# Performance work log

Measured on AMD Instinct MI355X. Metric: run time of the kernel, lower is better.

The kernel has to match this reference:

```python
import jax, jax.numpy as jnp
import numpy as np

N = 32768
H = 256

def setup_inputs() -> dict:
    key = jax.random.key(0)
    ks = jax.random.split(key, 8)
    def glorot(k, shape):
        fan_in, fan_out = shape
        s = jnp.sqrt(2.0 / (fan_in + fan_out)).astype(jnp.float32)
        return jax.random.normal(k, shape, dtype=jnp.float32) * s
    inp = {
        "x_norm": jax.random.normal(ks[0], (N, 3), dtype=jnp.float32),
        "nu": jnp.ones((1,), dtype=jnp.float32) * 0.01,
        "x_std": jnp.array([0.5, 0.5, 0.5], dtype=jnp.float32),
        "y_std": jnp.array([1.2, 1.2, 1.2, 0.8], dtype=jnp.float32),
        "W0": glorot(ks[1], (3, H)), "b0": jnp.zeros((H,), jnp.float32),
        "W1": glorot(ks[2], (H, H)), "b1": jnp.zeros((H,), jnp.float32),
        "W2": glorot(ks[3], (H, H)), "b2": jnp.zeros((H,), jnp.float32),
        "W3": glorot(ks[4], (H, H)), "b3": jnp.zeros((H,), jnp.float32),
        "W4": glorot(ks[5], (H, 4)), "b4": jnp.zeros((4,), jnp.float32),
    }
    return inp

def reference(x_norm, nu, x_std, y_std, W0, b0, W1, b1, W2, b2, W3, b3, W4, b4):
    # per-point MLP: R^3 -> R^4  (u, v, w, p)
    def f(x):
        h = jnp.tanh(x @ W0 + b0)
        h = jnp.tanh(h @ W1 + b1)
        h = jnp.tanh(h @ W2 + b2)
        h = jnp.tanh(h @ W3 + b3)
        return h @ W4 + b4  # [4]

    # Fused single-pass derivatives (replaces 13 autograd.grad calls):
    J = jax.vmap(jax.jacfwd(f))(x_norm)                 # [N,4,3] first derivs
    Hfull = jax.vmap(jax.jacfwd(jax.jacfwd(f)))(x_norm) # [N,4,3,3]
    Hdiag = jnp.diagonal(Hfull, axis1=2, axis2=3)       # [N,4,3] d2/dxi2 only

    # de-normalization scaling: y_std[y] / x_std[x]^order
    Js = J * y_std[None, :, None] / x_std[None, None, :]
    Hs = Hdiag * y_std[None, :, None] / (x_std[None, None, :] ** 2)

    continuity = Js[:, 0, 0] + Js[:, 1, 1] + Js[:, 2, 2]  # du/dx+dv/dy+dw/dz
    lap = Hs.sum(-1)                                       # [N,4] laplacians
    nu_s = nu[0]
    momentum_x = Js[:, 3, 0] - nu_s * lap[:, 0]
    momentum_y = Js[:, 3, 1] - nu_s * lap[:, 1]
    momentum_z = Js[:, 3, 2] - nu_s * lap[:, 2]

    phy_loss = continuity ** 2 + momentum_x ** 2 + momentum_y ** 2 + momentum_z ** 2
    return phy_loss  # [N], reduction='none' (already squeezed)
```

## Files before the change

### kernel.cpp

```cpp
#include <hip/hip_runtime.h>
#include <stdint.h>

typedef __attribute__((ext_vector_type(8))) _Float16 half8v;
typedef __attribute__((ext_vector_type(16))) float float16v;
typedef __attribute__((ext_vector_type(4))) float float4v;

#define NPTS_WG 32
#define NCH 5

__device__ __forceinline__ int agp(int c, int g, int p) {
    return ((c * 32 + g) * 32 + p) * 8;
}

__device__ __forceinline__ unsigned short f16b(float x) {
    const _Float16 h = (_Float16)x;
    return __builtin_bit_cast(unsigned short, h);
}

__device__ __forceinline__ uint32_t pk2f16(float a, float b) {
    return (uint32_t)f16b(a) | ((uint32_t)f16b(b) << 16);
}

__device__ __forceinline__ float fast_tanh(float z) {
    const float e = __expf(2.0f * z);
    return 1.0f - 2.0f / (e + 1.0f);
}

__global__ void wt_split_kernel(const float* __restrict__ W1, const float* __restrict__ W2,
                                const float* __restrict__ W3, unsigned short* __restrict__ wt)
{
    const int b = blockIdx.x;
    const int L = b >> 4;
    const int ch = b & 15;
    const int k0 = ch * 16;
    const float* W = (L == 0) ? W1 : (L == 1) ? W2 : W3;
    const int j = threadIdx.x;
    const int wv = j >> 5, l31 = j & 31;
    uint32_t hi[16], lo[16];
#pragma unroll
    for (int e = 0; e < 16; ++e) {
        const float x = W[(k0 + e) * 256 + j];
        const unsigned short h = f16b(x);
        const float hf = (float)__builtin_bit_cast(_Float16, h);
        hi[e] = h;
        lo[e] = f16b(x - hf);
    }
#pragma unroll
    for (int part = 0; part < 2; ++part) {
        const uint32_t* src = part ? lo : hi;
        unsigned short* base = wt +
            ((((size_t)(L * 2 + part) * 8 + wv) * 16 + ch) * 64) * 8;
#pragma unroll
        for (int hh = 0; hh < 2; ++hh) {
            uint4 v;
            const uint32_t* s = src + hh * 8;
            v.x = s[0] | (s[1] << 16);
            v.y = s[2] | (s[3] << 16);
            v.z = s[4] | (s[5] << 16);
            v.w = s[6] | (s[7] << 16);
            *(uint4*)(base + (hh * 32 + l31) * 8) = v;
        }
    }
}

__global__ __launch_bounds__(512, 4)
void pinn_mfma(const float* __restrict__ x_norm, const float* __restrict__ nu,
               const float* __restrict__ x_std, const float* __restrict__ y_std,
               const float* __restrict__ W0, const float* __restrict__ b0,
               const float* __restrict__ b1, const float* __restrict__ b2,
               const float* __restrict__ b3, const float* __restrict__ W4,
               const unsigned short* __restrict__ wt, float* __restrict__ out)
{
    __shared__ __align__(16) unsigned char smem[NCH * 32 * 256 * 2];
    unsigned short* AH = (unsigned short*)smem;
    float* part_lds = (float*)smem;
    float* y_lds = (float*)(smem + 16384);

    const int tid = threadIdx.x;
    const int lane = tid & 63;
    const int wv = tid >> 6;
    const int l31 = lane & 31;
    const int hh = lane >> 5;
    const int base_pt = blockIdx.x * NPTS_WG;

    const float xs0 = x_std[0], xs1 = x_std[1], xs2 = x_std[2];
    const float ixs20 = 1.f / (xs0 * xs0);
    const float ixs21 = 1.f / (xs1 * xs1);
    const float ixs22 = 1.f / (xs2 * xs2);

    {
        const int p = tid & 31;
        const int jq = tid >> 5;
        const float x0 = x_norm[(base_pt + p) * 3 + 0];
        const float x1 = x_norm[(base_pt + p) * 3 + 1];
        const float x2 = x_norm[(base_pt + p) * 3 + 2];
#pragma unroll
        for (int hf = 0; hf < 2; ++hf) {
            const int j8 = jq * 16 + hf * 8;
            const int g = 2 * jq + hf;
            float w0r[8], w1r[8], w2r[8], b0r[8];
            *(float4*)&w0r[0] = *(const float4*)&W0[0 * 256 + j8];
            *(float4*)&w0r[4] = *(const float4*)&W0[0 * 256 + j8 + 4];
            *(float4*)&w1r[0] = *(const float4*)&W0[1 * 256 + j8];
            *(float4*)&w1r[4] = *(const float4*)&W0[1 * 256 + j8 + 4];
            *(float4*)&w2r[0] = *(const float4*)&W0[2 * 256 + j8];
            *(float4*)&w2r[4] = *(const float4*)&W0[2 * 256 + j8 + 4];
            *(float4*)&b0r[0] = *(const float4*)&b0[j8];
            *(float4*)&b0r[4] = *(const float4*)&b0[j8 + 4];
            union { unsigned short u[8]; half8v v; } hv[NCH];
#pragma unroll
            for (int e = 0; e < 8; ++e) {
                const float z = b0r[e] + x0 * w0r[e] + x1 * w1r[e] + x2 * w2r[e];
                const float t = fast_tanh(z);
                const float s = 1.f - t * t;
                hv[0].u[e] = f16b(t);
                hv[1].u[e] = f16b(s * w0r[e]);
                hv[2].u[e] = f16b(s * w1r[e]);
                hv[3].u[e] = f16b(s * w2r[e]);
                hv[4].u[e] = f16b(-2.f * t * s *
                    (w0r[e] * w0r[e] * ixs20 + w1r[e] * w1r[e] * ixs21 +
                     w2r[e] * w2r[e] * ixs22));
            }
#pragma unroll
            for (int c = 0; c < NCH; ++c)
                *(half8v*)&AH[agp(c, g, p)] = hv[c].v;
        }
    }
    __syncthreads();

    const float* biases[3] = {b1, b2, b3};
    const int laneq = lane * 8;

#pragma unroll 1
    for (int L = 0; L < 3; ++L) {
        const unsigned short* whL = wt + ((size_t)(L * 2 + 0) * 8 + wv) * 8192 + laneq;
        const unsigned short* wlL = wt + ((size_t)(L * 2 + 1) * 8 + wv) * 8192 + laneq;
        float16v acc[NCH];
#pragma unroll
        for (int c = 0; c < NCH; ++c)
#pragma unroll
            for (int e = 0; e < 16; ++e) acc[c][e] = 0.f;

#pragma unroll
        for (int ch = 0; ch < 16; ++ch) {
            const half8v wh = *(const half8v*)(whL + ch * 512);
            const half8v wl = *(const half8v*)(wlL + ch * 512);
            half8v a[NCH];
            const int g = 2 * ch + hh;
#pragma unroll
            for (int c = 0; c < NCH; ++c)
                a[c] = *(const half8v*)&AH[agp(c, g, l31)];
            __builtin_amdgcn_s_setprio(1);
#pragma unroll
            for (int c = 0; c < NCH; ++c)
                acc[c] = __builtin_amdgcn_mfma_f32_32x32x16_f16(wh, a[c], acc[c], 0, 0, 0);
#pragma unroll
            for (int c = 0; c < 4; ++c)
                acc[c] = __builtin_amdgcn_mfma_f32_32x32x16_f16(wl, a[c], acc[c], 0, 0, 0);
            __builtin_amdgcn_s_setprio(0);
        }

        const float* bL = biases[L];
        __syncthreads();
#pragma unroll
        for (int q = 0; q < 4; ++q) {
            const int j0 = wv * 32 + 8 * q + 4 * hh;
            const int g = wv * 4 + q;
            float bj[4];
            *(float4*)&bj[0] = *(const float4*)&bL[j0];
            float val[NCH][4];
#pragma unroll
            for (int r = 0; r < 4; ++r) {
                const int e = q * 4 + r;
                const float z = acc[0][e] + bj[r];
                const float t = fast_tanh(z);
                const float s = 1.f - t * t;
                const float d1a = acc[1][e], d1b = acc[2][e], d1c = acc[3][e];
                val[0][r] = t;
                val[1][r] = s * d1a;
                val[2][r] = s * d1b;
                val[3][r] = s * d1c;
                val[4][r] = s * acc[4][e] - 2.f * t * s *
                    (d1a * d1a * ixs20 + d1b * d1b * ixs21 + d1c * d1c * ixs22);
            }
#pragma unroll
            for (int c = 0; c < NCH; ++c) {
                const uint32_t u0 = pk2f16(val[c][0], val[c][1]);
                const uint32_t u1 = pk2f16(val[c][2], val[c][3]);
                *(uint2*)&AH[agp(c, g, l31) + 4 * hh] = make_uint2(u0, u1);
            }
        }
        __syncthreads();
    }

    {
        const int l15 = lane & 15;
        const int g4 = lane >> 4;
        const int koct = wv * 32 + 8 * g4;
        const int gr = wv * 4 + g4;
        union { uint32_t u[4]; half8v v; } HB, LB;
#pragma unroll
        for (int i = 0; i < 4; ++i) {
            const float w0v = (l15 < 4) ? W4[(koct + 2 * i) * 4 + l15] : 0.f;
            const float w1v = (l15 < 4) ? W4[(koct + 2 * i + 1) * 4 + l15] : 0.f;
            const unsigned short h0 = f16b(w0v), h1 = f16b(w1v);
            const float r0 = w0v - (float)__builtin_bit_cast(_Float16, h0);
            const float r1 = w1v - (float)__builtin_bit_cast(_Float16, h1);
            HB.u[i] = (uint32_t)h0 | ((uint32_t)h1 << 16);
            LB.u[i] = (uint32_t)f16b(r0) | ((uint32_t)f16b(r1) << 16);
        }
        float4v acc4[4][2];
#pragma unroll
        for (int cc = 0; cc < 4; ++cc)
#pragma unroll
            for (int ph = 0; ph < 2; ++ph) acc4[cc][ph] = (float4v){0.f, 0.f, 0.f, 0.f};
#pragma unroll
        for (int cc = 0; cc < 4; ++cc) {
#pragma unroll
            for (int ph = 0; ph < 2; ++ph) {
                const half8v ah = *(const half8v*)&AH[agp(1 + cc, gr, l15 + 16 * ph)];
                acc4[cc][ph] = __builtin_amdgcn_mfma_f32_16x16x32_f16(HB.v, ah, acc4[cc][ph], 0, 0, 0);
                if (cc < 3)
                    acc4[cc][ph] = __builtin_amdgcn_mfma_f32_16x16x32_f16(LB.v, ah, acc4[cc][ph], 0, 0, 0);
            }
        }
        __syncthreads();
        if (g4 == 0) {
#pragma unroll
            for (int cc = 0; cc < 4; ++cc)
#pragma unroll
                for (int ph = 0; ph < 2; ++ph)
                    *(float4*)&part_lds[((wv * 4 + cc) * 32 + ph * 16 + l15) * 4] =
                        make_float4(acc4[cc][ph][0], acc4[cc][ph][1],
                                    acc4[cc][ph][2], acc4[cc][ph][3]);
        }
    }
    __syncthreads();

    {
        const int p = tid & 31;
        const int co = tid >> 5;
        const int o = co & 3;
        const int c4 = co >> 2;
        float sum = 0.f;
#pragma unroll
        for (int w8 = 0; w8 < 8; ++w8)
            sum += part_lds[((w8 * 4 + c4) * 32 + p) * 4 + o];
        const float scale = (c4 < 3) ? (y_std[o] / x_std[c4]) : y_std[o];
        y_lds[co * 32 + p] = sum * scale;
    }
    __syncthreads();

    if (tid < 32) {
        const int p = tid;
        const float nuv = nu[0];
        #define YV(c4, o) y_lds[(((c4) * 4) + (o)) * 32 + p]
        const float cont = YV(0, 0) + YV(1, 1) + YV(2, 2);
        const float mx = YV(0, 3) - nuv * YV(3, 0);
        const float my = YV(1, 3) - nuv * YV(3, 1);
        const float mz = YV(2, 3) - nuv * YV(3, 2);
        out[base_pt + p] = cont * cont + mx * mx + my * my + mz * mz;
        #undef YV
    }
}

extern "C" void kernel_launch(void* const* d_in, const int* in_sizes, int n_in,
                              void* d_out, int out_size, void* d_ws, size_t ws_size,
                              hipStream_t stream)
{
    const float* x_norm = (const float*)d_in[0];
    const float* nu     = (const float*)d_in[1];
    const float* x_std  = (const float*)d_in[2];
    const float* y_std  = (const float*)d_in[3];
    const float* W0 = (const float*)d_in[4];  const float* b0 = (const float*)d_in[5];
    const float* W1 = (const float*)d_in[6];  const float* b1 = (const float*)d_in[7];
    const float* W2 = (const float*)d_in[8];  const float* b2 = (const float*)d_in[9];
    const float* W3 = (const float*)d_in[10]; const float* b3 = (const float*)d_in[11];
    const float* W4 = (const float*)d_in[12];
    (void)n_in; (void)out_size; (void)ws_size;
    unsigned short* wt = (unsigned short*)d_ws;
    float* out = (float*)d_out;
    const int npts = in_sizes[0] / 3;

    wt_split_kernel<<<48, 256, 0, stream>>>(W1, W2, W3, wt);
    pinn_mfma<<<npts / NPTS_WG, 512, 0, stream>>>(x_norm, nu, x_std, y_std,
        W0, b0, b1, b2, b3, W4, wt, out);
}
```

Measured before the change: 147.3 us.

## Use 16 waves per block with 16x16x32 MFMA tiles for hidden layers

Doubles the workgroup to 1024 threads so each of 16 waves owns a 16-column output slice, switching hidden-layer GEMMs from 32x32x16 to 16x16x32 MFMA and re-laying out the pre-split fp16 weights to match. The goal is more waves in flight to hide LDS and MFMA latency and to cut per-wave accumulator registers. In exchange, each wave now loads A operands twice per k-step and issues twice as many MFMAs. The waves beyond the first eight sit idle during the output-layer stage.

```diff
diff --git a/kernel.cpp b/kernel.cpp
--- a/kernel.cpp
+++ b/kernel.cpp
@@ -2,7 +2,6 @@
 #include <stdint.h>
 
 typedef __attribute__((ext_vector_type(8))) _Float16 half8v;
-typedef __attribute__((ext_vector_type(16))) float float16v;
 typedef __attribute__((ext_vector_type(4))) float float4v;
 
 #define NPTS_WG 32
@@ -31,11 +30,12 @@
 {
     const int b = blockIdx.x;
     const int L = b >> 4;
-    const int ch = b & 15;
-    const int k0 = ch * 16;
+    const int strip = b & 15;
+    const int k0 = strip * 16;
     const float* W = (L == 0) ? W1 : (L == 1) ? W2 : W3;
     const int j = threadIdx.x;
-    const int wv = j >> 5, l31 = j & 31;
+    const int wave = j >> 4, l15 = j & 15;
+    const int kstep = strip >> 1;
     uint32_t hi[16], lo[16];
 #pragma unroll
     for (int e = 0; e < 16; ++e) {
@@ -49,21 +49,23 @@
     for (int part = 0; part < 2; ++part) {
         const uint32_t* src = part ? lo : hi;
         unsigned short* base = wt +
-            ((((size_t)(L * 2 + part) * 8 + wv) * 16 + ch) * 64) * 8;
-#pragma unroll
-        for (int hh = 0; hh < 2; ++hh) {
+            (((size_t)(L * 2 + part) * 16 + wave) * 8 + kstep) * 512;
+#pragma unroll
+        for (int half = 0; half < 2; ++half) {
+            const int k = k0 + half * 8;
+            const int g4 = (k >> 3) & 3;
+            const uint32_t* s = src + half * 8;
             uint4 v;
-            const uint32_t* s = src + hh * 8;
             v.x = s[0] | (s[1] << 16);
             v.y = s[2] | (s[3] << 16);
             v.z = s[4] | (s[5] << 16);
             v.w = s[6] | (s[7] << 16);
-            *(uint4*)(base + (hh * 32 + l31) * 8) = v;
-        }
-    }
-}
-
-__global__ __launch_bounds__(512, 4)
+            *(uint4*)(base + (g4 * 16 + l15) * 8) = v;
+        }
+    }
+}
+
+__global__ __launch_bounds__(1024, 4)
 void pinn_mfma(const float* __restrict__ x_norm, const float* __restrict__ nu,
                const float* __restrict__ x_std, const float* __restrict__ y_std,
                const float* __restrict__ W0, const float* __restrict__ b0,
@@ -79,8 +81,8 @@
     const int tid = threadIdx.x;
     const int lane = tid & 63;
     const int wv = tid >> 6;
-    const int l31 = lane & 31;
-    const int hh = lane >> 5;
+    const int l15 = lane & 15;
+    const int g4 = lane >> 4;
     const int base_pt = blockIdx.x * NPTS_WG;
 
     const float xs0 = x_std[0], xs1 = x_std[1], xs2 = x_std[2];
@@ -91,40 +93,36 @@
     {
         const int p = tid & 31;
         const int jq = tid >> 5;
+        const int j8 = jq * 8;
         const float x0 = x_norm[(base_pt + p) * 3 + 0];
         const float x1 = x_norm[(base_pt + p) * 3 + 1];
         const float x2 = x_norm[(base_pt + p) * 3 + 2];
-#pragma unroll
-        for (int hf = 0; hf < 2; ++hf) {
-            const int j8 = jq * 16 + hf * 8;
-            const int g = 2 * jq + hf;
-            float w0r[8], w1r[8], w2r[8], b0r[8];
-            *(float4*)&w0r[0] = *(const float4*)&W0[0 * 256 + j8];
-            *(float4*)&w0r[4] = *(const float4*)&W0[0 * 256 + j8 + 4];
-            *(float4*)&w1r[0] = *(const float4*)&W0[1 * 256 + j8];
-            *(float4*)&w1r[4] = *(const float4*)&W0[1 * 256 + j8 + 4];
-            *(float4*)&w2r[0] = *(const float4*)&W0[2 * 256 + j8];
-            *(float4*)&w2r[4] = *(const float4*)&W0[2 * 256 + j8 + 4];
-            *(float4*)&b0r[0] = *(const float4*)&b0[j8];
-            *(float4*)&b0r[4] = *(const float4*)&b0[j8 + 4];
-            union { unsigned short u[8]; half8v v; } hv[NCH];
-#pragma unroll
-            for (int e = 0; e < 8; ++e) {
-                const float z = b0r[e] + x0 * w0r[e] + x1 * w1r[e] + x2 * w2r[e];
-                const float t = fast_tanh(z);
-                const float s = 1.f - t * t;
-                hv[0].u[e] = f16b(t);
-                hv[1].u[e] = f16b(s * w0r[e]);
-                hv[2].u[e] = f16b(s * w1r[e]);
-                hv[3].u[e] = f16b(s * w2r[e]);
-                hv[4].u[e] = f16b(-2.f * t * s *
-                    (w0r[e] * w0r[e] * ixs20 + w1r[e] * w1r[e] * ixs21 +
-                     w2r[e] * w2r[e] * ixs22));
-            }
-#pragma unroll
-            for (int c = 0; c < NCH; ++c)
-                *(half8v*)&AH[agp(c, g, p)] = hv[c].v;
-        }
+        float w0r[8], w1r[8], w2r[8], b0r[8];
+        *(float4*)&w0r[0] = *(const float4*)&W0[0 * 256 + j8];
+        *(float4*)&w0r[4] = *(const float4*)&W0[0 * 256 + j8 + 4];
+        *(float4*)&w1r[0] = *(const float4*)&W0[1 * 256 + j8];
+        *(float4*)&w1r[4] = *(const float4*)&W0[1 * 256 + j8 + 4];
+        *(float4*)&w2r[0] = *(const float4*)&W0[2 * 256 + j8];
+        *(float4*)&w2r[4] = *(const float4*)&W0[2 * 256 + j8 + 4];
+        *(float4*)&b0r[0] = *(const float4*)&b0[j8];
+        *(float4*)&b0r[4] = *(const float4*)&b0[j8 + 4];
+        union { unsigned short u[8]; half8v v; } hv[NCH];
+#pragma unroll
+        for (int e = 0; e < 8; ++e) {
+            const float z = b0r[e] + x0 * w0r[e] + x1 * w1r[e] + x2 * w2r[e];
+            const float t = fast_tanh(z);
+            const float s = 1.f - t * t;
+            hv[0].u[e] = f16b(t);
+            hv[1].u[e] = f16b(s * w0r[e]);
+            hv[2].u[e] = f16b(s * w1r[e]);
+            hv[3].u[e] = f16b(s * w2r[e]);
+            hv[4].u[e] = f16b(-2.f * t * s *
+                (w0r[e] * w0r[e] * ixs20 + w1r[e] * w1r[e] * ixs21 +
+                 w2r[e] * w2r[e] * ixs22));
+        }
+#pragma unroll
+        for (int c = 0; c < NCH; ++c)
+            *(half8v*)&AH[agp(c, jq, p)] = hv[c].v;
     }
     __syncthreads();
 
@@ -133,69 +131,76 @@
 
 #pragma unroll 1
     for (int L = 0; L < 3; ++L) {
-        const unsigned short* whL = wt + ((size_t)(L * 2 + 0) * 8 + wv) * 8192 + laneq;
-        const unsigned short* wlL = wt + ((size_t)(L * 2 + 1) * 8 + wv) * 8192 + laneq;
-        float16v acc[NCH];
+        const unsigned short* whL = wt + (((size_t)(L * 2 + 0) * 16 + wv) * 8) * 512 + laneq;
+        const unsigned short* wlL = wt + (((size_t)(L * 2 + 1) * 16 + wv) * 8) * 512 + laneq;
+        float4v acc[NCH][2];
 #pragma unroll
         for (int c = 0; c < NCH; ++c)
 #pragma unroll
-            for (int e = 0; e < 16; ++e) acc[c][e] = 0.f;
-
-#pragma unroll
-        for (int ch = 0; ch < 16; ++ch) {
-            const half8v wh = *(const half8v*)(whL + ch * 512);
-            const half8v wl = *(const half8v*)(wlL + ch * 512);
-            half8v a[NCH];
-            const int g = 2 * ch + hh;
-#pragma unroll
-            for (int c = 0; c < NCH; ++c)
-                a[c] = *(const half8v*)&AH[agp(c, g, l31)];
+            for (int ph = 0; ph < 2; ++ph) acc[c][ph] = (float4v){0.f, 0.f, 0.f, 0.f};
+
+#pragma unroll
+        for (int ks = 0; ks < 8; ++ks) {
+            const half8v wh = *(const half8v*)(whL + ks * 512);
+            const half8v wl = *(const half8v*)(wlL + ks * 512);
+            const int g = ks * 4 + g4;
+            half8v a0[NCH], a1[NCH];
+#pragma unroll
+            for (int c = 0; c < NCH; ++c) {
+                a0[c] = *(const half8v*)&AH[agp(c, g, l15)];
+                a1[c] = *(const half8v*)&AH[agp(c, g, l15 + 16)];
+            }
             __builtin_amdgcn_s_setprio(1);
 #pragma unroll
-            for (int c = 0; c < NCH; ++c)
-                acc[c] = __builtin_amdgcn_mfma_f32_32x32x16_f16(wh, a[c], acc[c], 0, 0, 0);
-#pragma unroll
-            for (int c = 0; c < 4; ++c)
-                acc[c] = __builtin_amdgcn_mfma_f32_32x32x16_f16(wl, a[c], acc[c], 0, 0, 0);
+            for (int c = 0; c < NCH; ++c) {
+                acc[c][0] = __builtin_amdgcn_mfma_f32_16x16x32_f16(wh, a0[c], acc[c][0], 0, 0, 0);
+                acc[c][1] = __builtin_amdgcn_mfma_f32_16x16x32_f16(wh, a1[c], acc[c][1], 0, 0, 0);
+            }
+#pragma unroll
+            for (int c = 0; c < 4; ++c) {
+                acc[c][0] = __builtin_amdgcn_mfma_f32_16x16x32_f16(wl, a0[c], acc[c][0], 0, 0, 0);
+                acc[c][1] = __builtin_amdgcn_mfma_f32_16x16x32_f16(wl, a1[c], acc[c][1], 0, 0, 0);
+            }
             __builtin_amdgcn_s_setprio(0);
         }
 
         const float* bL = biases[L];
         __syncthreads();
-#pragma unroll
-        for (int q = 0; q < 4; ++q) {
-            const int j0 = wv * 32 + 8 * q + 4 * hh;
-            const int g = wv * 4 + q;
+        {
+            const int j0 = wv * 16 + g4 * 4;
+            const int g = wv * 2 + (g4 >> 1);
+            const int off = (g4 & 1) * 4;
             float bj[4];
             *(float4*)&bj[0] = *(const float4*)&bL[j0];
-            float val[NCH][4];
-#pragma unroll
-            for (int r = 0; r < 4; ++r) {
-                const int e = q * 4 + r;
-                const float z = acc[0][e] + bj[r];
-                const float t = fast_tanh(z);
-                const float s = 1.f - t * t;
-                const float d1a = acc[1][e], d1b = acc[2][e], d1c = acc[3][e];
-                val[0][r] = t;
-                val[1][r] = s * d1a;
-                val[2][r] = s * d1b;
-                val[3][r] = s * d1c;
-                val[4][r] = s * acc[4][e] - 2.f * t * s *
-                    (d1a * d1a * ixs20 + d1b * d1b * ixs21 + d1c * d1c * ixs22);
-            }
-#pragma unroll
-            for (int c = 0; c < NCH; ++c) {
-                const uint32_t u0 = pk2f16(val[c][0], val[c][1]);
-                const uint32_t u1 = pk2f16(val[c][2], val[c][3]);
-                *(uint2*)&AH[agp(c, g, l31) + 4 * hh] = make_uint2(u0, u1);
-            }
-        }
-        __syncthreads();
-    }
-
-    {
-        const int l15 = lane & 15;
-        const int g4 = lane >> 4;
+#pragma unroll
+            for (int ph = 0; ph < 2; ++ph) {
+                const int p = l15 + 16 * ph;
+                float val[NCH][4];
+#pragma unroll
+                for (int r = 0; r < 4; ++r) {
+                    const float z = acc[0][ph][r] + bj[r];
+                    const float t = fast_tanh(z);
+                    const float s = 1.f - t * t;
+                    const float d1a = acc[1][ph][r], d1b = acc[2][ph][r], d1c = acc[3][ph][r];
+                    val[0][r] = t;
+                    val[1][r] = s * d1a;
+                    val[2][r] = s * d1b;
+                    val[3][r] = s * d1c;
+                    val[4][r] = s * acc[4][ph][r] - 2.f * t * s *
+                        (d1a * d1a * ixs20 + d1b * d1b * ixs21 + d1c * d1c * ixs22);
+                }
+#pragma unroll
+                for (int c = 0; c < NCH; ++c) {
+                    const uint32_t u0 = pk2f16(val[c][0], val[c][1]);
+                    const uint32_t u1 = pk2f16(val[c][2], val[c][3]);
+                    *(uint2*)&AH[agp(c, g, p) + off] = make_uint2(u0, u1);
+                }
+            }
+        }
+        __syncthreads();
+    }
+
+    if (wv < 8) {
         const int koct = wv * 32 + 8 * g4;
         const int gr = wv * 4 + g4;
         union { uint32_t u[4]; half8v v; } HB, LB;
@@ -234,10 +239,12 @@
                         make_float4(acc4[cc][ph][0], acc4[cc][ph][1],
                                     acc4[cc][ph][2], acc4[cc][ph][3]);
         }
+    } else {
+        __syncthreads();
     }
     __syncthreads();
 
-    {
+    if (tid < 512) {
         const int p = tid & 31;
         const int co = tid >> 5;
         const int o = co & 3;
@@ -283,6 +290,6 @@
     const int npts = in_sizes[0] / 3;
 
     wt_split_kernel<<<48, 256, 0, stream>>>(W1, W2, W3, wt);
-    pinn_mfma<<<npts / NPTS_WG, 512, 0, stream>>>(x_norm, nu, x_std, y_std,
+    pinn_mfma<<<npts / NPTS_WG, 1024, 0, stream>>>(x_norm, nu, x_std, y_std,
         W0, b0, b1, b2, b3, W4, wt, out);
 }
```

Result: slower. 330.4 us (+124.3%).
